# Kernel tuning notes

Hardware: AMD Instinct MI355X
Metric: run time of the kernel (lower is better)

Reference implementation:

```python
import jax, jax.numpy as jnp
import numpy as np

N = 2048
IN_DIM = 256
OUT_DIM = 64
N_HEADS = 8  # head_dim == n_heads required by a: Linear(2*n_heads, 1)
NEG_BIG = -9.0e15


def setup_inputs() -> dict:
    key = jax.random.key(0)
    k1, k2, k3, k4 = jax.random.split(key, 4)
    h = jax.random.normal(k1, (N, IN_DIM), dtype=jnp.float32)
    adj = jax.random.randint(k2, (N, N), 0, 2, dtype=jnp.int32)
    # xavier_uniform with gain=1.414 for W: bound = gain*sqrt(6/(fan_in+fan_out))
    bw = 1.414 * np.sqrt(6.0 / (IN_DIM + OUT_DIM))
    W_w = jax.random.uniform(k3, (OUT_DIM, IN_DIM), minval=-bw, maxval=bw, dtype=jnp.float32)
    W_b = jnp.zeros((OUT_DIM,), dtype=jnp.float32)
    ba = 1.414 * np.sqrt(6.0 / (2 * N_HEADS + 1))
    a_w = jax.random.uniform(k4, (1, 2 * N_HEADS), minval=-ba, maxval=ba, dtype=jnp.float32)
    a_b = jnp.zeros((1,), dtype=jnp.float32)
    return {"h": h, "adj": adj, "W_w": W_w, "W_b": W_b, "a_w": a_w, "a_b": a_b}


def reference(h, adj, W_w, W_b, a_w, a_b):
    H = a_w.shape[1] // 2
    out_dim = W_w.shape[0]
    Dh = out_dim // H  # == H by construction
    n = h.shape[0]
    wh = h @ W_w.T + W_b                      # [N, out_dim]
    wh_head = wh.reshape(n, H, Dh)            # [N, H, Dh]
    aL = a_w[0, :Dh]                           # applies to source node i features
    aR = a_w[0, Dh:]                           # applies to node j features
    e_i = jnp.einsum('nhd,d->nh', wh_head, aL)  # [N, H]
    e_j = jnp.einsum('nhd,d->nh', wh_head, aR)  # [N, H]
    # scores[i,j,h] without materializing the N*N concat tensor
    scores = e_i[:, None, :] + e_j[None, :, :] + a_b[0]   # [N, N, H]
    scores = jnp.where(scores >= 0, scores, 0.2 * scores)  # leaky_relu(0.2)
    masked = jnp.where(adj[:, :, None] > 0, scores, NEG_BIG)
    att = jax.nn.softmax(masked, axis=1)       # normalize over j
    # out[h,i,d] = sum_j att[i,j,h] * wh_head[j,h,d]
    out = jnp.einsum('ijh,jhd->hid', att, wh_head)  # [H, N, Dh]
    out = jax.nn.elu(out)
    return out.reshape(-1, out_dim)            # faithful to .view(-1, out_dim)
```

## Files before the change

kernel.cpp:

```cpp
#include <hip/hip_runtime.h>
#include <math.h>

#define NN 2048
#define INDIM 256
#define ODIM 64
#define NH 8
#define DHD 8
#define LOG2E 1.44269504088896340736f
#define JSPLIT 4
#define JCHUNK (NN / JSPLIT)
#define IBLK 4

__global__ __launch_bounds__(256) void gat_pre(
    const float* __restrict__ h, const float* __restrict__ Ww,
    const float* __restrict__ Wb, const float* __restrict__ aw,
    const float* __restrict__ ab,
    unsigned short* __restrict__ whb, float* __restrict__ eiL,
    float* __restrict__ ejL)
{
    __shared__ float sH[IBLK][INDIM];
    const int t = threadIdx.x;
    const int n0 = blockIdx.x * 4;
    ((float4*)&sH[0][0])[t] = ((const float4*)(h + (size_t)n0 * INDIM))[t];
    __syncthreads();

    const int o  = t & 63;
    const int wv = t >> 6;
    const int n  = n0 + wv;
    const float4* w4 = (const float4*)(Ww + (size_t)o * INDIM);
    float acc = 0.f;
#pragma unroll 8
    for (int k = 0; k < INDIM / 4; ++k) {
        const float4 wk = w4[k];
        const float4 hv = *(const float4*)&sH[wv][k * 4];
        acc = fmaf(wk.x, hv.x, acc); acc = fmaf(wk.y, hv.y, acc);
        acc = fmaf(wk.z, hv.z, acc); acc = fmaf(wk.w, hv.w, acc);
    }
    acc += Wb[o];

    {
        unsigned int u = __float_as_uint(acc);
        unsigned int r = (u + 0x7FFF + ((u >> 16) & 1)) >> 16;
        whb[(size_t)n * ODIM + o] = (unsigned short)r;
    }

    const int d = o & 7;
    float pi = acc * aw[d];
    float pj = acc * aw[NH + d];
    pi += __shfl_xor(pi, 1, 64); pj += __shfl_xor(pj, 1, 64);
    pi += __shfl_xor(pi, 2, 64); pj += __shfl_xor(pj, 2, 64);
    pi += __shfl_xor(pi, 4, 64); pj += __shfl_xor(pj, 4, 64);
    if (d == 0) {
        const int hd = o >> 3;
        eiL[n * NH + hd] = (pi + ab[0]) * LOG2E;
        ejL[n * NH + hd] = pj * LOG2E;
    }
}

__global__ __launch_bounds__(512) void gat_main(
    const int* __restrict__ adj, const unsigned short* __restrict__ whb,
    const float* __restrict__ eiL, const float* __restrict__ ejL,
    float* __restrict__ pacc, float* __restrict__ pden)
{
    __shared__ unsigned char s_bits[JCHUNK];
    __shared__ float s_red[8][8][IBLK][9];
    const int t  = threadIdx.x;
    const int i0 = (blockIdx.x >> 2) * IBLK;
    const int js = blockIdx.x & 3;
    const int jbase = js * JCHUNK;

    {
        unsigned int b = 0;
#pragma unroll
        for (int i = 0; i < IBLK; ++i)
            b |= (adj[(size_t)(i0 + i) * NN + jbase + t] != 0) << i;
        s_bits[t] = (unsigned char)b;
    }
    __syncthreads();

    const int hh = t & 7;
    const int jj = t >> 3;
    float eih[IBLK];
#pragma unroll
    for (int i = 0; i < IBLK; ++i) eih[i] = eiL[(i0 + i) * NH + hh];

    float den[IBLK] = {0.f, 0.f, 0.f, 0.f};
    float acc[IBLK][DHD];
#pragma unroll
    for (int i = 0; i < IBLK; ++i)
#pragma unroll
        for (int d = 0; d < DHD; ++d) acc[i][d] = 0.f;

#pragma unroll 2
    for (int it = 0; it < JCHUNK / 64; ++it) {
        const int jl = it * 64 + jj;
        const int j  = jbase + jl;
        const float ejv = ejL[j * NH + hh];
        const uint4 wd = ((const uint4*)whb)[j * NH + hh];
        const int bits = s_bits[jl];

        float e[IBLK];
#pragma unroll
        for (int i = 0; i < IBLK; ++i) {
            float s = eih[i] + ejv;
            s = fmaxf(s, 0.2f * s);
            s = (bits & (1 << i)) ? s : -192.0f;
            e[i] = __builtin_amdgcn_exp2f(s);
            den[i] += e[i];
        }
#pragma unroll
        for (int q = 0; q < 4; ++q) {
            const unsigned int w = (&wd.x)[q];
            const float lo = __uint_as_float(w << 16);
            const float hi = __uint_as_float(w & 0xFFFF0000u);
#pragma unroll
            for (int i = 0; i < IBLK; ++i) {
                acc[i][2 * q]     = fmaf(e[i], lo, acc[i][2 * q]);
                acc[i][2 * q + 1] = fmaf(e[i], hi, acc[i][2 * q + 1]);
            }
        }
    }

#pragma unroll
    for (int m = 8; m <= 32; m <<= 1) {
#pragma unroll
        for (int i = 0; i < IBLK; ++i) {
            den[i] += __shfl_xor(den[i], m, 64);
#pragma unroll
            for (int d = 0; d < DHD; ++d)
                acc[i][d] += __shfl_xor(acc[i][d], m, 64);
        }
    }
    const int lane = t & 63;
    const int wv   = t >> 6;
    if (lane < 8) {
#pragma unroll
        for (int i = 0; i < IBLK; ++i) {
#pragma unroll
            for (int d = 0; d < DHD; ++d) s_red[wv][lane][i][d] = acc[i][d];
            s_red[wv][lane][i][8] = den[i];
        }
    }
    __syncthreads();

    {
        const int i  = (t >> 7) & 3;
        const int hD = (t >> 4) & 7;
        const int sl = t & 15;
        if (sl < 9) {
            float v = 0.f;
#pragma unroll
            for (int w2 = 0; w2 < 8; ++w2) v += s_red[w2][hD][i][sl];
            if (sl < 8)
                pacc[(((size_t)js * NN + i0 + i) * NH + hD) * DHD + sl] = v;
            else
                pden[((size_t)js * NN + i0 + i) * NH + hD] = v;
        }
    }
}

__global__ __launch_bounds__(256) void gat_fin(
    const float* __restrict__ pacc, const float* __restrict__ pden,
    float* __restrict__ out)
{
    const int gid = blockIdx.x * 256 + threadIdx.x;
    const int d = gid & 7;
    const int hD = (gid >> 3) & 7;
    const int i = gid >> 6;
    float v = 0.f, dn = 0.f;
#pragma unroll
    for (int js = 0; js < JSPLIT; ++js) {
        v  += pacc[(((size_t)js * NN + i) * NH + hD) * DHD + d];
        dn += pden[((size_t)js * NN + i) * NH + hD];
    }
    float r = v / dn;
    r = (r > 0.f) ? r : expm1f(r);
    out[(size_t)hD * (NN * DHD) + (size_t)i * DHD + d] = r;
}

extern "C" void kernel_launch(void* const* d_in, const int* in_sizes, int n_in,
                              void* d_out, int out_size, void* d_ws, size_t ws_size,
                              hipStream_t stream) {
    const float* h   = (const float*)d_in[0];
    const int*   adj = (const int*)d_in[1];
    const float* Ww  = (const float*)d_in[2];
    const float* Wb  = (const float*)d_in[3];
    const float* aw  = (const float*)d_in[4];
    const float* ab  = (const float*)d_in[5];
    float* out = (float*)d_out;

    char* ws = (char*)d_ws;
    unsigned short* whb = (unsigned short*)ws;
    float* eiL  = (float*)(ws + 262144);
    float* ejL  = (float*)(ws + 327680);
    float* pacc = (float*)(ws + 393216);
    float* pden = (float*)(ws + 2490368);

    gat_pre<<<NN / 4, 256, 0, stream>>>(h, Ww, Wb, aw, ab, whb, eiL, ejL);
    gat_main<<<(NN / IBLK) * JSPLIT, 512, 0, stream>>>(adj, whb, eiL, ejL, pacc, pden);
    gat_fin<<<NN * ODIM / 256, 256, 0, stream>>>(pacc, pden, out);
}
```

Measured before the change: 49.29 us.

## Drop j-split, fuse finalize into main kernel, prefetch and vectorize loads

Removes the four-way split over j, so each block processes all 2048 neighbours for its 4 rows and applies the softmax normalisation and ELU directly. This eliminates the partial-sum buffers and the third kernel launch. Adjacency rows are now read as int4 vectors, and the next iteration's e_j and bf16 features are software-prefetched into registers. The trade-off is a grid cut from 2048 to 512 blocks of 512 threads, with longer serial loops per block, which may lower parallelism on a 256-CU device.

```diff
diff --git a/kernel.cpp b/kernel.cpp
--- a/kernel.cpp
+++ b/kernel.cpp
@@ -7,8 +7,6 @@
 #define NH 8
 #define DHD 8
 #define LOG2E 1.44269504088896340736f
-#define JSPLIT 4
-#define JCHUNK (NN / JSPLIT)
 #define IBLK 4
 
 __global__ __launch_bounds__(256) void gat_pre(
@@ -60,21 +58,25 @@
 __global__ __launch_bounds__(512) void gat_main(
     const int* __restrict__ adj, const unsigned short* __restrict__ whb,
     const float* __restrict__ eiL, const float* __restrict__ ejL,
-    float* __restrict__ pacc, float* __restrict__ pden)
+    float* __restrict__ out)
 {
-    __shared__ unsigned char s_bits[JCHUNK];
+    __shared__ unsigned char s_bits[NN];
     __shared__ float s_red[8][8][IBLK][9];
     const int t  = threadIdx.x;
-    const int i0 = (blockIdx.x >> 2) * IBLK;
-    const int js = blockIdx.x & 3;
-    const int jbase = js * JCHUNK;
+    const int i0 = blockIdx.x * IBLK;
 
     {
-        unsigned int b = 0;
+        unsigned int b0 = 0, b1 = 0, b2 = 0, b3 = 0;
 #pragma unroll
-        for (int i = 0; i < IBLK; ++i)
-            b |= (adj[(size_t)(i0 + i) * NN + jbase + t] != 0) << i;
-        s_bits[t] = (unsigned char)b;
+        for (int i = 0; i < IBLK; ++i) {
+            const int4 v = *(const int4*)(adj + (size_t)(i0 + i) * NN + 4 * t);
+            b0 |= (v.x != 0) << i;
+            b1 |= (v.y != 0) << i;
+            b2 |= (v.z != 0) << i;
+            b3 |= (v.w != 0) << i;
+        }
+        ((uchar4*)s_bits)[t] = make_uchar4((unsigned char)b0, (unsigned char)b1,
+                                           (unsigned char)b2, (unsigned char)b3);
     }
     __syncthreads();
 
@@ -91,18 +93,26 @@
 #pragma unroll
         for (int d = 0; d < DHD; ++d) acc[i][d] = 0.f;
 
+    const float* ejp = ejL + jj * NH + hh;
+    const uint4* wp  = (const uint4*)whb + jj * NH + hh;
+    const unsigned char* bp = s_bits + jj;
+
+    float pe = *ejp;
+    uint4 pw = *wp;
+
 #pragma unroll 2
-    for (int it = 0; it < JCHUNK / 64; ++it) {
-        const int jl = it * 64 + jj;
-        const int j  = jbase + jl;
-        const float ejv = ejL[j * NH + hh];
-        const uint4 wd = ((const uint4*)whb)[j * NH + hh];
-        const int bits = s_bits[jl];
+    for (int it = 0; it < NN / 64; ++it) {
+        const float ce = pe;
+        const uint4 cw = pw;
+        const int bits = *bp;
+        ejp += 64 * NH; wp += 64 * NH; bp += 64;
+        pe = *ejp;
+        pw = *wp;
 
         float e[IBLK];
 #pragma unroll
         for (int i = 0; i < IBLK; ++i) {
-            float s = eih[i] + ejv;
+            float s = eih[i] + ce;
             s = fmaxf(s, 0.2f * s);
             s = (bits & (1 << i)) ? s : -192.0f;
             e[i] = __builtin_amdgcn_exp2f(s);
@@ -110,7 +120,7 @@
         }
 #pragma unroll
         for (int q = 0; q < 4; ++q) {
-            const unsigned int w = (&wd.x)[q];
+            const unsigned int w = (&cw.x)[q];
             const float lo = __uint_as_float(w << 16);
             const float hi = __uint_as_float(w & 0xFFFF0000u);
 #pragma unroll
@@ -143,39 +153,20 @@
     }
     __syncthreads();
 
-    {
-        const int i  = (t >> 7) & 3;
-        const int hD = (t >> 4) & 7;
-        const int sl = t & 15;
-        if (sl < 9) {
-            float v = 0.f;
+    if (t < 256) {
+        const int i  = t >> 6;
+        const int hD = (t >> 3) & 7;
+        const int d  = t & 7;
+        float v = 0.f, dn = 0.f;
 #pragma unroll
-            for (int w2 = 0; w2 < 8; ++w2) v += s_red[w2][hD][i][sl];
-            if (sl < 8)
-                pacc[(((size_t)js * NN + i0 + i) * NH + hD) * DHD + sl] = v;
-            else
-                pden[((size_t)js * NN + i0 + i) * NH + hD] = v;
+        for (int w2 = 0; w2 < 8; ++w2) {
+            v  += s_red[w2][hD][i][d];
+            dn += s_red[w2][hD][i][8];
         }
+        float r = v / dn;
+        r = (r > 0.f) ? r : expm1f(r);
+        out[(size_t)hD * (NN * DHD) + (size_t)(i0 + i) * DHD + d] = r;
     }
-}
-
-__global__ __launch_bounds__(256) void gat_fin(
-    const float* __restrict__ pacc, const float* __restrict__ pden,
-    float* __restrict__ out)
-{
-    const int gid = blockIdx.x * 256 + threadIdx.x;
-    const int d = gid & 7;
-    const int hD = (gid >> 3) & 7;
-    const int i = gid >> 6;
-    float v = 0.f, dn = 0.f;
-#pragma unroll
-    for (int js = 0; js < JSPLIT; ++js) {
-        v  += pacc[(((size_t)js * NN + i) * NH + hD) * DHD + d];
-        dn += pden[((size_t)js * NN + i) * NH + hD];
-    }
-    float r = v / dn;
-    r = (r > 0.f) ? r : expm1f(r);
-    out[(size_t)hD * (NN * DHD) + (size_t)i * DHD + d] = r;
 }
 
 extern "C" void kernel_launch(void* const* d_in, const int* in_sizes, int n_in,
@@ -193,10 +184,7 @@
     unsigned short* whb = (unsigned short*)ws;
     float* eiL  = (float*)(ws + 262144);
     float* ejL  = (float*)(ws + 327680);
-    float* pacc = (float*)(ws + 393216);
-    float* pden = (float*)(ws + 2490368);
 
     gat_pre<<<NN / 4, 256, 0, stream>>>(h, Ww, Wb, aw, ab, whb, eiL, ejL);
-    gat_main<<<(NN / IBLK) * JSPLIT, 512, 0, stream>>>(adj, whb, eiL, ejL, pacc, pden);
-    gat_fin<<<NN * ODIM / 256, 256, 0, stream>>>(pacc, pden, out);
+    gat_main<<<NN / IBLK, 512, 0, stream>>>(adj, whb, eiL, ejL, out);
 }
```

Result: faster. 43.14 us (-12.5%).
